# Kernel tuning notes

Hardware: AMD Instinct MI355X
Metric: run time of the kernel (lower is better)

The kernel has to match this reference:

```python
import jax, jax.numpy as jnp
import numpy as np

W_SIZE = 7
K = 15
EPS = 1e-8  # torch cosine_similarity eps


def setup_inputs() -> dict:
    key = jax.random.key(0)
    k0, k1, k2 = jax.random.split(key, 3)
    dim = 128
    return {
        "x_in": jax.random.normal(k0, (4, dim, 112, 112), dtype=jnp.float32),
        "f_w": jax.random.normal(k1, (dim // 8, dim), dtype=jnp.float32) * (1.0 / np.sqrt(dim)),
        "f_b": jax.random.normal(k2, (dim // 8,), dtype=jnp.float32) * 0.01,
        "edge_alpha": jnp.ones((1,), dtype=jnp.float32),
        "edge_beta": jnp.zeros((1,), dtype=jnp.float32),
    }


def reference(x_in, f_w, f_b, edge_alpha, edge_beta):
    B, C, H, W = x_in.shape
    Wg = Hg = W_SIZE
    w, h = H // Wg, W // Hg
    N = w * h
    # patchify: b c (Wg w) (Hg h) -> (b Wg Hg) c w h
    xp = x_in.reshape(B, C, Wg, w, Hg, h).transpose(0, 2, 4, 1, 3, 5).reshape(B * Wg * Hg, C, w, h)
    P = xp.shape[0]
    # 1x1 conv f: C -> C//8 channels
    f = jnp.einsum('pcwh,dc->pdwh', xp, f_w) + f_b[None, :, None, None]
    Cf = f.shape[1]
    x_flat = f.reshape(P, Cf, N).transpose(0, 2, 1)  # [P, N, Cf]
    # normalized spatial grid (torch std is unbiased -> ddof=1)
    gi, gj = jnp.meshgrid(jnp.arange(w, dtype=jnp.float32), jnp.arange(h, dtype=jnp.float32), indexing='ij')
    grid = jnp.stack([gi, gj], axis=-1).reshape(N, 2)
    grid = (grid - grid.mean(0)) / (grid.std(0, ddof=1) + 1e-5)
    x_aug = jnp.concatenate([x_flat, jnp.broadcast_to(grid[None], (P, N, 2))], axis=-1)  # [P,N,Cf+2]
    # pairwise cosine similarity via normalized dot products
    nrm = jnp.maximum(jnp.linalg.norm(x_aug, axis=-1, keepdims=True), EPS)
    xn = x_aug / nrm
    sim = jnp.einsum('pnd,pmd->pnm', xn, xn)  # [P,N,N]
    topv, topi = jax.lax.top_k(sim, K)        # [P,N,K]
    # edge weights; scatter_softmax over row index == softmax over k (each row has exactly K edges)
    weights = jax.nn.sigmoid(edge_beta[0] + edge_alpha[0] * topv)
    wn = jax.nn.softmax(weights, axis=-1)     # [P,N,K]
    # gather original-channel messages from top-k neighbors and aggregate
    xo = xp.reshape(P, C, N).transpose(0, 2, 1)                 # [P,N,C]
    gathered = jax.vmap(lambda xr, ir: xr[ir])(xo, topi)        # [P,N,K,C]
    out_flat = jnp.einsum('pnk,pnkc->pnc', wn, gathered)        # [P,N,C]
    out = out_flat.reshape(P, w, h, C).transpose(0, 3, 1, 2)    # [P,C,w,h]
    # un-patchify: (b Wg Hg) c w h -> b c (Wg w) (Hg h)
    out = out.reshape(B, Wg, Hg, C, w, h).transpose(0, 3, 1, 4, 2, 5).reshape(B, C, H, W)
    return out
```

## Files before the change

### kernel.cpp

```cpp
#include <hip/hip_runtime.h>
#include <math.h>

#define KSEL 15
#define CIN 128
#define CF 16
#define HH 112
#define PLANE 12544
#define NN 256
#define ROWSTRIDE 20

static __device__ __forceinline__ unsigned mono32(float f) {
    unsigned u = __float_as_uint(f);
    return ((int)u < 0) ? ~u : (u | 0x80000000u);
}
static __device__ __forceinline__ float demono32(unsigned u) {
    return ((int)u < 0) ? __uint_as_float(u & 0x7FFFFFFFu) : __uint_as_float(~u);
}

__global__ __launch_bounds__(256) void k1_features(
    const float* __restrict__ x, const float* __restrict__ fw, const float* __restrict__ fb,
    double* __restrict__ xa64, float* __restrict__ xa32, unsigned* __restrict__ dirtyCount)
{
    __shared__ float lfw[CIN * CF];
    __shared__ float lfb[CF];
    const int tid = threadIdx.x;
    if (blockIdx.x == 0 && tid == 0) *dirtyCount = 0u;
    const int p  = blockIdx.x >> 2;
    const int n0 = (blockIdx.x & 3) * 64;
    const int b = p / 49, g = p % 49;
    const int gI = g / 7, gJ = g % 7;
    const float* xb = x + (size_t)b * CIN * PLANE + (size_t)(gI * 16 * HH + gJ * 16);

    for (int q = tid; q < CIN * CF; q += 256) { int d = q >> 7, c = q & 127; lfw[c * CF + d] = fw[q]; }
    if (tid < CF) lfb[tid] = fb[tid];
    __syncthreads();

    const int nl = tid >> 2, dq = tid & 3;
    const int n = n0 + nl, i = n >> 4, j = n & 15;
    const float* xp = xb + i * HH + j;

    double a0 = 0.0, a1 = 0.0, a2 = 0.0, a3 = 0.0;
#pragma unroll 4
    for (int c = 0; c < CIN; ++c) {
        double xc = (double)xp[(size_t)c * PLANE];
        float4 wv = *(const float4*)&lfw[c * CF + dq * 4];
        a0 = fma(xc, (double)wv.x, a0);
        a1 = fma(xc, (double)wv.y, a1);
        a2 = fma(xc, (double)wv.z, a2);
        a3 = fma(xc, (double)wv.w, a3);
    }
    a0 += (double)lfb[dq * 4 + 0];
    a1 += (double)lfb[dq * 4 + 1];
    a2 += (double)lfb[dq * 4 + 2];
    a3 += (double)lfb[dq * 4 + 3];

    const double GDIV = 4.618802153517006 + 1e-5;
    double gx = ((double)i - 7.5) / GDIV;
    double gy = ((double)j - 7.5) / GDIV;

    double ss = a0 * a0;
    ss = fma(a1, a1, ss); ss = fma(a2, a2, ss); ss = fma(a3, a3, ss);
    if (dq == 3) { ss = fma(gx, gx, ss); ss = fma(gy, gy, ss); }
    ss += __shfl_xor(ss, 1);
    ss += __shfl_xor(ss, 2);
    double nrm = fmax(sqrt(ss), 1e-8);

    size_t ro = ((size_t)p * NN + n) * ROWSTRIDE;
    double o0 = a0 / nrm, o1 = a1 / nrm, o2 = a2 / nrm, o3 = a3 / nrm;
    xa64[ro + dq * 4 + 0] = o0; xa64[ro + dq * 4 + 1] = o1;
    xa64[ro + dq * 4 + 2] = o2; xa64[ro + dq * 4 + 3] = o3;
    xa32[ro + dq * 4 + 0] = (float)o0; xa32[ro + dq * 4 + 1] = (float)o1;
    xa32[ro + dq * 4 + 2] = (float)o2; xa32[ro + dq * 4 + 3] = (float)o3;
    if (dq == 3) {
        double g0 = gx / nrm, g1 = gy / nrm;
        xa64[ro + 16] = g0; xa64[ro + 17] = g1; xa64[ro + 18] = 0.0; xa64[ro + 19] = 0.0;
        xa32[ro + 16] = (float)g0; xa32[ro + 17] = (float)g1; xa32[ro + 18] = 0.f; xa32[ro + 19] = 0.f;
    }
}

__global__ __launch_bounds__(256) void k2_select(
    const float* __restrict__ xa32,
    const float* __restrict__ ea, const float* __restrict__ eb,
    int* __restrict__ topi, float* __restrict__ wkout,
    unsigned* __restrict__ dirtyCount, int* __restrict__ dirtyList)
{
    __shared__ float tile[NN * ROWSTRIDE];
    __shared__ unsigned kv[NN * 17];
    const int tid = threadIdx.x;
    const int p = blockIdx.x >> 4, sub = blockIdx.x & 15;

    const float* src = xa32 + (size_t)p * NN * ROWSTRIDE;
#pragma unroll
    for (int q = 0; q < 5; ++q) {
        int idx = q * 256 + tid;
        ((float4*)tile)[idx] = ((const float4*)src)[idx];
    }
    __syncthreads();

    const int lane = tid & 15;
    const int grp  = tid >> 4;
    const int rip  = sub * 16 + grp;
    const int row  = p * NN + rip;

    float xr[18];
#pragma unroll
    for (int d = 0; d < 18; ++d) xr[d] = tile[rip * ROWSTRIDE + d];

    unsigned k[16];
#pragma unroll
    for (int s = 0; s < 16; ++s) {
        int m = s * 16 + lane;
        const float4* xm4 = (const float4*)&tile[m * ROWSTRIDE];
        float bb[18];
        *(float4*)&bb[0]  = xm4[0];
        *(float4*)&bb[4]  = xm4[1];
        *(float4*)&bb[8]  = xm4[2];
        *(float4*)&bb[12] = xm4[3];
        *(float2*)&bb[16] = *(const float2*)&tile[m * ROWSTRIDE + 16];
        float acc = 0.f;
#pragma unroll
        for (int d = 0; d < 18; ++d) acc = fmaf(xr[d], bb[d], acc);
        k[s] = (mono32(acc) & 0xFFFFFF00u) | (unsigned)(255 - m);
    }

#pragma unroll
    for (int kk = 2; kk <= 16; kk <<= 1) {
#pragma unroll
        for (int jj = kk >> 1; jj > 0; jj >>= 1) {
#pragma unroll
            for (int ii = 0; ii < 16; ++ii) {
                int ll = ii ^ jj;
                if (ll > ii) {
                    bool up = ((ii & kk) == 0);
                    unsigned a = k[ii], bbv = k[ll];
                    bool sw = up ? (a > bbv) : (a < bbv);
                    k[ii] = sw ? bbv : a; k[ll] = sw ? a : bbv;
                }
            }
        }
    }
#pragma unroll
    for (int s = 0; s < 16; ++s) kv[tid * 17 + s] = k[s];

    int ptr = 15;
    unsigned mycand = 0;
    unsigned myhead = k[15];
#pragma unroll
    for (int e = 0; e < 16; ++e) {
        unsigned W = myhead;
        unsigned o;
        o = __shfl_xor(W, 1);  W = (o > W) ? o : W;
        o = __shfl_xor(W, 2);  W = (o > W) ? o : W;
        o = __shfl_xor(W, 4);  W = (o > W) ? o : W;
        o = __shfl_xor(W, 8);  W = (o > W) ? o : W;
        if (lane == e) mycand = W;
        bool won = (myhead == W);
        ptr -= won ? 1 : 0;
        int rp = ptr < 0 ? 0 : ptr;
        unsigned reread = kv[tid * 17 + rp];
        myhead = won ? reread : myhead;
    }

    unsigned v15 = __shfl(mycand, 14, 16);
    unsigned v16 = __shfl(mycand, 15, 16);
    float lo = demono32(v15 & 0xFFFFFF00u) - 1e-5f;
    float hi = demono32((v16 & 0xFFFFFF00u) + 0x100u) + 1e-5f;
    bool dirty = !(hi < lo);
    if (lane == 0 && dirty) {
        unsigned slot = atomicAdd(dirtyCount, 1u);
        dirtyList[slot] = row;
    }

    int mym = 255 - (int)(mycand & 0xFFu);
    float sv = demono32(mycand & 0xFFFFFF00u);
    float alpha = ea[0], beta = eb[0];
    float sg = 1.f / (1.f + expf(-(beta + alpha * sv)));
    float v = (lane < KSEL) ? sg : -1e30f;
    float mx = v, of;
    of = __shfl_xor(mx, 1); mx = fmaxf(mx, of);
    of = __shfl_xor(mx, 2); mx = fmaxf(mx, of);
    of = __shfl_xor(mx, 4); mx = fmaxf(mx, of);
    of = __shfl_xor(mx, 8); mx = fmaxf(mx, of);
    float ex = expf(v - mx);
    float sm = ex;
    of = __shfl_xor(sm, 1); sm += of;
    of = __shfl_xor(sm, 2); sm += of;
    of = __shfl_xor(sm, 4); sm += of;
    of = __shfl_xor(sm, 8); sm += of;

    topi[row * 16 + lane] = mym;
    wkout[row * 16 + lane] = (lane < KSEL) ? (ex / sm) : 0.f;
}

__global__ __launch_bounds__(64) void k2b_dirty(
    const double* __restrict__ xa64, const float* __restrict__ ea, const float* __restrict__ eb,
    const unsigned* __restrict__ dirtyCount, const int* __restrict__ dirtyList,
    int* __restrict__ topi, float* __restrict__ wkout)
{
    const int nd = (int)*dirtyCount;
    const int lane = threadIdx.x;
    for (int idx = blockIdx.x; idx < nd; idx += gridDim.x) {
        const int row = dirtyList[idx];
        const int p = row >> 8;
        const double* xr64 = xa64 + (size_t)row * ROWSTRIDE;

        double sv[4]; int smi[4];
#pragma unroll
        for (int s4 = 0; s4 < 4; ++s4) {
            int m = s4 * 64 + lane;
            const double* xm64 = xa64 + ((size_t)p * NN + m) * ROWSTRIDE;
            double s = 0.0;
#pragma unroll
            for (int d = 0; d < 18; ++d) s = fma(xr64[d], xm64[d], s);
            sv[s4] = s; smi[s4] = m;
        }

        double cv = -3.0; int cm = 0;
#pragma unroll
        for (int e = 0; e < KSEL; ++e) {
            double lv = sv[0]; int lm = smi[0];
#pragma unroll
            for (int s4 = 1; s4 < 4; ++s4) {
                bool t = (sv[s4] > lv) || (sv[s4] == lv && smi[s4] < lm);
                lv = t ? sv[s4] : lv; lm = t ? smi[s4] : lm;
            }
#pragma unroll
            for (int off = 1; off < 64; off <<= 1) {
                double ov = __shfl_xor(lv, off);
                int    om = __shfl_xor(lm, off);
                bool t = (ov > lv) || (ov == lv && om < lm);
                lv = t ? ov : lv; lm = t ? om : lm;
            }
            if (lane == e) { cv = lv; cm = lm; }
#pragma unroll
            for (int s4 = 0; s4 < 4; ++s4) if (smi[s4] == lm) sv[s4] = -3.0;
        }

        float alpha = ea[0], beta = eb[0];
        float sg = 1.f / (1.f + expf(-(beta + alpha * (float)cv)));
        float v = (lane < KSEL) ? sg : -1e30f;
        float mx = v, of;
        for (int off = 1; off < 64; off <<= 1) { of = __shfl_xor(mx, off); mx = fmaxf(mx, of); }
        float ex = expf(v - mx);
        float sm = ex;
        for (int off = 1; off < 64; off <<= 1) { of = __shfl_xor(sm, off); sm += of; }
        float w = ex / sm;
        if (lane < 16) {
            topi[row * 16 + lane] = (lane < KSEL) ? cm : 0;
            wkout[row * 16 + lane] = (lane < KSEL) ? w : 0.f;
        }
    }
}

__global__ __launch_bounds__(256) void k3_aggregate(
    const float* __restrict__ x, const int* __restrict__ topi, const float* __restrict__ wk,
    float* __restrict__ out)
{
    __shared__ float tile[NN * ROWSTRIDE];
    const int tid = threadIdx.x;
    const int pb = blockIdx.x >> 3, cg = blockIdx.x & 7, c0 = cg * 16;
    const int b = pb / 49, g = pb % 49;
    const int gI = g / 7, gJ = g % 7;
    const float* xb = x + ((size_t)b * CIN + c0) * PLANE + (size_t)(gI * 16 * HH + gJ * 16);

#pragma unroll
    for (int rep = 0; rep < 4; ++rep) {
        int linear = rep * 256 + tid;
        int cc = linear >> 6, chunk = linear & 63;
        int pos = chunk * 4, ii = pos >> 4, jj = pos & 15;
        float4 v = *(const float4*)(xb + (size_t)cc * PLANE + ii * HH + jj);
        tile[(pos + 0) * ROWSTRIDE + cc] = v.x;
        tile[(pos + 1) * ROWSTRIDE + cc] = v.y;
        tile[(pos + 2) * ROWSTRIDE + cc] = v.z;
        tile[(pos + 3) * ROWSTRIDE + cc] = v.w;
    }
    __syncthreads();

    const int n = tid;
    const int row = pb * NN + n;
    float acc[16];
#pragma unroll
    for (int c = 0; c < 16; ++c) acc[c] = 0.f;

#pragma unroll
    for (int kq = 0; kq < 4; ++kq) {
        int4   mi4 = ((const int4*)(topi + (size_t)row * 16))[kq];
        float4 w4  = ((const float4*)(wk  + (size_t)row * 16))[kq];
        const int   mis[4] = { mi4.x, mi4.y, mi4.z, mi4.w };
        const float ws4[4] = { w4.x, w4.y, w4.z, w4.w };
#pragma unroll
        for (int u = 0; u < 4; ++u) {
            float w = ws4[u];
            const float4* sp = (const float4*)&tile[mis[u] * ROWSTRIDE];
#pragma unroll
            for (int q = 0; q < 4; ++q) {
                float4 f = sp[q];
                acc[q * 4 + 0] = fmaf(w, f.x, acc[q * 4 + 0]);
                acc[q * 4 + 1] = fmaf(w, f.y, acc[q * 4 + 1]);
                acc[q * 4 + 2] = fmaf(w, f.z, acc[q * 4 + 2]);
                acc[q * 4 + 3] = fmaf(w, f.w, acc[q * 4 + 3]);
            }
        }
    }
    const int ii = n >> 4, jj = n & 15;
    float* ob = out + ((size_t)b * CIN + c0) * PLANE + (size_t)(gI * 16 * HH + gJ * 16) + ii * HH + jj;
#pragma unroll
    for (int cc = 0; cc < 16; ++cc) ob[(size_t)cc * PLANE] = acc[cc];
}

extern "C" void kernel_launch(void* const* d_in, const int* in_sizes, int n_in,
                              void* d_out, int out_size, void* d_ws, size_t ws_size,
                              hipStream_t stream) {
    const float* x  = (const float*)d_in[0];
    const float* fw = (const float*)d_in[1];
    const float* fb = (const float*)d_in[2];
    const float* ea = (const float*)d_in[3];
    const float* eb = (const float*)d_in[4];
    float* out = (float*)d_out;

    int nB = in_sizes[0] / (CIN * PLANE);
    int nP = nB * 49;
    size_t nRows = (size_t)nP * NN;

    char* wsb = (char*)d_ws;
    size_t off = 0;
    auto carve = [&](size_t bytes) { char* r = wsb + off; off = (off + bytes + 255) & ~(size_t)255; return r; };
    double*   xa64   = (double*)  carve(nRows * ROWSTRIDE * sizeof(double));
    float*    xa32   = (float*)   carve(nRows * ROWSTRIDE * sizeof(float));
    int*      topi   = (int*)     carve(nRows * 16 * sizeof(int));
    float*    wk     = (float*)   carve(nRows * 16 * sizeof(float));
    unsigned* dcnt   = (unsigned*)carve(256);
    int*      dlist  = (int*)     carve(nRows * sizeof(int));

    hipLaunchKernelGGL(k1_features, dim3(nP * 4), dim3(256), 0, stream, x, fw, fb, xa64, xa32, dcnt);
    hipLaunchKernelGGL(k2_select,   dim3(nP * 16), dim3(256), 0, stream, xa32, ea, eb, topi, wk, dcnt, dlist);
    hipLaunchKernelGGL(k2b_dirty,   dim3(256), dim3(64), 0, stream, xa64, ea, eb, dcnt, dlist, topi, wk);
    hipLaunchKernelGGL(k3_aggregate, dim3(nP * 8), dim3(256), 0, stream, x, topi, wk, out);
}
```

Measured before the change: 156.7 us.

## Register-block similarity computation in select kernel and split k1 FMA chains

The select kernel now computes a 4x4 register tile of dot products per thread, reusing each loaded row across four rows and four columns, and stages the keys through shared memory in a padded layout. Each lane then reads a contiguous run of 16 keys, and the merge re-read comes from registers via a select chain instead of shared memory. In the feature kernel the double-precision accumulation is split into even and odd chains to shorten dependency latency. The changes add a barrier and more register pressure in exchange for fewer shared-memory loads per FMA. The per-lane candidate set changes from strided columns to contiguous ones, but the result is equivalent.

```diff
diff --git a/kernel.cpp b/kernel.cpp
--- a/kernel.cpp
+++ b/kernel.cpp
@@ -8,6 +8,7 @@
 #define PLANE 12544
 #define NN 256
 #define ROWSTRIDE 20
+#define KVSTRIDE 260
 
 static __device__ __forceinline__ unsigned mono32(float f) {
     unsigned u = __float_as_uint(f);
@@ -39,20 +40,27 @@
     const int n = n0 + nl, i = n >> 4, j = n & 15;
     const float* xp = xb + i * HH + j;
 
-    double a0 = 0.0, a1 = 0.0, a2 = 0.0, a3 = 0.0;
-#pragma unroll 4
-    for (int c = 0; c < CIN; ++c) {
-        double xc = (double)xp[(size_t)c * PLANE];
-        float4 wv = *(const float4*)&lfw[c * CF + dq * 4];
-        a0 = fma(xc, (double)wv.x, a0);
-        a1 = fma(xc, (double)wv.y, a1);
-        a2 = fma(xc, (double)wv.z, a2);
-        a3 = fma(xc, (double)wv.w, a3);
-    }
-    a0 += (double)lfb[dq * 4 + 0];
-    a1 += (double)lfb[dq * 4 + 1];
-    a2 += (double)lfb[dq * 4 + 2];
-    a3 += (double)lfb[dq * 4 + 3];
+    double e0 = 0.0, e1 = 0.0, e2 = 0.0, e3 = 0.0;
+    double o0 = 0.0, o1 = 0.0, o2 = 0.0, o3 = 0.0;
+#pragma unroll 2
+    for (int c = 0; c < CIN; c += 2) {
+        double xc0 = (double)xp[(size_t)c * PLANE];
+        double xc1 = (double)xp[(size_t)(c + 1) * PLANE];
+        float4 wv0 = *(const float4*)&lfw[c * CF + dq * 4];
+        float4 wv1 = *(const float4*)&lfw[(c + 1) * CF + dq * 4];
+        e0 = fma(xc0, (double)wv0.x, e0);
+        e1 = fma(xc0, (double)wv0.y, e1);
+        e2 = fma(xc0, (double)wv0.z, e2);
+        e3 = fma(xc0, (double)wv0.w, e3);
+        o0 = fma(xc1, (double)wv1.x, o0);
+        o1 = fma(xc1, (double)wv1.y, o1);
+        o2 = fma(xc1, (double)wv1.z, o2);
+        o3 = fma(xc1, (double)wv1.w, o3);
+    }
+    double a0 = e0 + o0 + (double)lfb[dq * 4 + 0];
+    double a1 = e1 + o1 + (double)lfb[dq * 4 + 1];
+    double a2 = e2 + o2 + (double)lfb[dq * 4 + 2];
+    double a3 = e3 + o3 + (double)lfb[dq * 4 + 3];
 
     const double GDIV = 4.618802153517006 + 1e-5;
     double gx = ((double)i - 7.5) / GDIV;
@@ -66,11 +74,11 @@
     double nrm = fmax(sqrt(ss), 1e-8);
 
     size_t ro = ((size_t)p * NN + n) * ROWSTRIDE;
-    double o0 = a0 / nrm, o1 = a1 / nrm, o2 = a2 / nrm, o3 = a3 / nrm;
-    xa64[ro + dq * 4 + 0] = o0; xa64[ro + dq * 4 + 1] = o1;
-    xa64[ro + dq * 4 + 2] = o2; xa64[ro + dq * 4 + 3] = o3;
-    xa32[ro + dq * 4 + 0] = (float)o0; xa32[ro + dq * 4 + 1] = (float)o1;
-    xa32[ro + dq * 4 + 2] = (float)o2; xa32[ro + dq * 4 + 3] = (float)o3;
+    double f0 = a0 / nrm, f1 = a1 / nrm, f2 = a2 / nrm, f3 = a3 / nrm;
+    xa64[ro + dq * 4 + 0] = f0; xa64[ro + dq * 4 + 1] = f1;
+    xa64[ro + dq * 4 + 2] = f2; xa64[ro + dq * 4 + 3] = f3;
+    xa32[ro + dq * 4 + 0] = (float)f0; xa32[ro + dq * 4 + 1] = (float)f1;
+    xa32[ro + dq * 4 + 2] = (float)f2; xa32[ro + dq * 4 + 3] = (float)f3;
     if (dq == 3) {
         double g0 = gx / nrm, g1 = gy / nrm;
         xa64[ro + 16] = g0; xa64[ro + 17] = g1; xa64[ro + 18] = 0.0; xa64[ro + 19] = 0.0;
@@ -85,7 +93,7 @@
     unsigned* __restrict__ dirtyCount, int* __restrict__ dirtyList)
 {
     __shared__ float tile[NN * ROWSTRIDE];
-    __shared__ unsigned kv[NN * 17];
+    __shared__ unsigned kv[16 * KVSTRIDE];
     const int tid = threadIdx.x;
     const int p = blockIdx.x >> 4, sub = blockIdx.x & 15;
 
@@ -97,30 +105,65 @@
     }
     __syncthreads();
 
-    const int lane = tid & 15;
-    const int grp  = tid >> 4;
-    const int rip  = sub * 16 + grp;
-    const int row  = p * NN + rip;
-
-    float xr[18];
-#pragma unroll
-    for (int d = 0; d < 18; ++d) xr[d] = tile[rip * ROWSTRIDE + d];
+    const int w    = tid >> 6;
+    const int lane = tid & 63;
+    const int r0   = sub * 16 + w * 4;
+    const int m0   = lane * 4;
+
+    float xr[4][18];
+#pragma unroll
+    for (int rr = 0; rr < 4; ++rr) {
+        const float4* xp4 = (const float4*)&tile[(r0 + rr) * ROWSTRIDE];
+        float4 x0 = xp4[0], x1 = xp4[1], x2 = xp4[2], x3 = xp4[3];
+        float2 xt = *(const float2*)&tile[(r0 + rr) * ROWSTRIDE + 16];
+        xr[rr][0]=x0.x; xr[rr][1]=x0.y; xr[rr][2]=x0.z; xr[rr][3]=x0.w;
+        xr[rr][4]=x1.x; xr[rr][5]=x1.y; xr[rr][6]=x1.z; xr[rr][7]=x1.w;
+        xr[rr][8]=x2.x; xr[rr][9]=x2.y; xr[rr][10]=x2.z; xr[rr][11]=x2.w;
+        xr[rr][12]=x3.x; xr[rr][13]=x3.y; xr[rr][14]=x3.z; xr[rr][15]=x3.w;
+        xr[rr][16]=xt.x; xr[rr][17]=xt.y;
+    }
+
+    unsigned keys[4][4];
+#pragma unroll
+    for (int mm = 0; mm < 4; ++mm) {
+        const int m = m0 + mm;
+        const float4* bp4 = (const float4*)&tile[m * ROWSTRIDE];
+        float4 b0 = bp4[0], b1 = bp4[1], b2 = bp4[2], b3 = bp4[3];
+        float2 bt = *(const float2*)&tile[m * ROWSTRIDE + 16];
+#pragma unroll
+        for (int rr = 0; rr < 4; ++rr) {
+            float s = 0.f;
+            s = fmaf(xr[rr][0],  b0.x, s); s = fmaf(xr[rr][1],  b0.y, s);
+            s = fmaf(xr[rr][2],  b0.z, s); s = fmaf(xr[rr][3],  b0.w, s);
+            s = fmaf(xr[rr][4],  b1.x, s); s = fmaf(xr[rr][5],  b1.y, s);
+            s = fmaf(xr[rr][6],  b1.z, s); s = fmaf(xr[rr][7],  b1.w, s);
+            s = fmaf(xr[rr][8],  b2.x, s); s = fmaf(xr[rr][9],  b2.y, s);
+            s = fmaf(xr[rr][10], b2.z, s); s = fmaf(xr[rr][11], b2.w, s);
+            s = fmaf(xr[rr][12], b3.x, s); s = fmaf(xr[rr][13], b3.y, s);
+            s = fmaf(xr[rr][14], b3.z, s); s = fmaf(xr[rr][15], b3.w, s);
+            s = fmaf(xr[rr][16], bt.x, s); s = fmaf(xr[rr][17], bt.y, s);
+            keys[rr][mm] = (mono32(s) & 0xFFFFFF00u) | (unsigned)(255 - m);
+        }
+    }
+#pragma unroll
+    for (int rr = 0; rr < 4; ++rr) {
+        uint4 kw = make_uint4(keys[rr][0], keys[rr][1], keys[rr][2], keys[rr][3]);
+        *(uint4*)&kv[(w * 4 + rr) * KVSTRIDE + m0] = kw;
+    }
+    __syncthreads();
+
+    const int l16 = tid & 15;
+    const int rb  = tid >> 4;
+    const int row = p * NN + sub * 16 + rb;
 
     unsigned k[16];
-#pragma unroll
-    for (int s = 0; s < 16; ++s) {
-        int m = s * 16 + lane;
-        const float4* xm4 = (const float4*)&tile[m * ROWSTRIDE];
-        float bb[18];
-        *(float4*)&bb[0]  = xm4[0];
-        *(float4*)&bb[4]  = xm4[1];
-        *(float4*)&bb[8]  = xm4[2];
-        *(float4*)&bb[12] = xm4[3];
-        *(float2*)&bb[16] = *(const float2*)&tile[m * ROWSTRIDE + 16];
-        float acc = 0.f;
-#pragma unroll
-        for (int d = 0; d < 18; ++d) acc = fmaf(xr[d], bb[d], acc);
-        k[s] = (mono32(acc) & 0xFFFFFF00u) | (unsigned)(255 - m);
+    {
+        const uint4* kp = (const uint4*)&kv[rb * KVSTRIDE + l16 * 16];
+        uint4 q0 = kp[0], q1 = kp[1], q2 = kp[2], q3 = kp[3];
+        k[0]=q0.x; k[1]=q0.y; k[2]=q0.z; k[3]=q0.w;
+        k[4]=q1.x; k[5]=q1.y; k[6]=q1.z; k[7]=q1.w;
+        k[8]=q2.x; k[9]=q2.y; k[10]=q2.z; k[11]=q2.w;
+        k[12]=q3.x; k[13]=q3.y; k[14]=q3.z; k[15]=q3.w;
     }
 
 #pragma unroll
@@ -139,12 +182,10 @@
             }
         }
     }
-#pragma unroll
-    for (int s = 0; s < 16; ++s) kv[tid * 17 + s] = k[s];
 
     int ptr = 15;
+    unsigned myhead = k[15];
     unsigned mycand = 0;
-    unsigned myhead = k[15];
 #pragma unroll
     for (int e = 0; e < 16; ++e) {
         unsigned W = myhead;
@@ -153,12 +194,14 @@
         o = __shfl_xor(W, 2);  W = (o > W) ? o : W;
         o = __shfl_xor(W, 4);  W = (o > W) ? o : W;
         o = __shfl_xor(W, 8);  W = (o > W) ? o : W;
-        if (lane == e) mycand = W;
+        if (l16 == e) mycand = W;
         bool won = (myhead == W);
         ptr -= won ? 1 : 0;
         int rp = ptr < 0 ? 0 : ptr;
-        unsigned reread = kv[tid * 17 + rp];
-        myhead = won ? reread : myhead;
+        unsigned nh = k[0];
+#pragma unroll
+        for (int ii = 1; ii < 16; ++ii) nh = (rp == ii) ? k[ii] : nh;
+        myhead = won ? nh : myhead;
     }
 
     unsigned v15 = __shfl(mycand, 14, 16);
@@ -166,7 +209,7 @@
     float lo = demono32(v15 & 0xFFFFFF00u) - 1e-5f;
     float hi = demono32((v16 & 0xFFFFFF00u) + 0x100u) + 1e-5f;
     bool dirty = !(hi < lo);
-    if (lane == 0 && dirty) {
+    if (l16 == 0 && dirty) {
         unsigned slot = atomicAdd(dirtyCount, 1u);
         dirtyList[slot] = row;
     }
@@ -175,7 +218,7 @@
     float sv = demono32(mycand & 0xFFFFFF00u);
     float alpha = ea[0], beta = eb[0];
     float sg = 1.f / (1.f + expf(-(beta + alpha * sv)));
-    float v = (lane < KSEL) ? sg : -1e30f;
+    float v = (l16 < KSEL) ? sg : -1e30f;
     float mx = v, of;
     of = __shfl_xor(mx, 1); mx = fmaxf(mx, of);
     of = __shfl_xor(mx, 2); mx = fmaxf(mx, of);
@@ -188,8 +231,8 @@
     of = __shfl_xor(sm, 4); sm += of;
     of = __shfl_xor(sm, 8); sm += of;
 
-    topi[row * 16 + lane] = mym;
-    wkout[row * 16 + lane] = (lane < KSEL) ? (ex / sm) : 0.f;
+    topi[row * 16 + l16] = mym;
+    wkout[row * 16 + l16] = (l16 < KSEL) ? (ex / sm) : 0.f;
 }
 
 __global__ __launch_bounds__(64) void k2b_dirty(
```

Measured after the change: 173.2 us. 10.5% more time.
